# Performance work log

Hardware: AMD Instinct MI355X
Metric: run time of the kernel (lower is better)

## Reference

```python
import jax, jax.numpy as jnp
import numpy as np

D_MODEL = 1024
D_FFN = 4096
H = 16
D_HEAD = D_MODEL // H
B, L = 2, 2048
EPS = 1e-6


def layer_norm(x, a, b):
    # Matches torch: std is unbiased (ddof=1), and divides by (std + eps)
    mean = jnp.mean(x, axis=-1, keepdims=True)
    var = jnp.sum((x - mean) ** 2, axis=-1, keepdims=True) / (x.shape[-1] - 1)
    std = jnp.sqrt(var)
    return (x - mean) / (std + EPS) * a + b


def setup_inputs() -> dict:
    key = jax.random.key(0)
    ks = jax.random.split(key, 10)
    s = 0.02
    x = jax.random.normal(ks[0], (B, L, D_MODEL), dtype=jnp.float32)
    mask = jnp.tril(jnp.ones((L, L), dtype=jnp.int32))[None, None]  # causal [1,1,L,L]
    return {
        "x": x,
        "mask": mask,
        "Wqkv": jax.random.normal(ks[1], (D_MODEL, 3 * D_MODEL), jnp.float32) * s,
        "bqkv": jnp.zeros((3 * D_MODEL,), jnp.float32),
        "Wo": jax.random.normal(ks[2], (D_MODEL, D_MODEL), jnp.float32) * s,
        "bo": jnp.zeros((D_MODEL,), jnp.float32),
        "W1": jax.random.normal(ks[3], (D_MODEL, D_FFN), jnp.float32) * s,
        "b1": jnp.zeros((D_FFN,), jnp.float32),
        "W2": jax.random.normal(ks[4], (D_FFN, D_MODEL), jnp.float32) * s,
        "b2": jnp.zeros((D_MODEL,), jnp.float32),
        "ln1_a": jnp.ones((D_MODEL,), jnp.float32),
        "ln1_b": jnp.zeros((D_MODEL,), jnp.float32),
        "ln2_a": jnp.ones((D_MODEL,), jnp.float32),
        "ln2_b": jnp.zeros((D_MODEL,), jnp.float32),
    }


def reference(x, mask, Wqkv, bqkv, Wo, bo, W1, b1, W2, b2, ln1_a, ln1_b, ln2_a, ln2_b):
    b, l, d = x.shape
    # --- attention sublayer ---
    qkv = x @ Wqkv + bqkv                                   # [b, l, 3*d]
    qkv = qkv.reshape(b, l, 3, H, D_HEAD)                   # '(three h d)' ordering
    q, k, v = qkv[:, :, 0], qkv[:, :, 1], qkv[:, :, 2]      # each [b, l, h, dh]
    scores = jnp.einsum('bqhd,bkhd->bhqk', q, k) / jnp.sqrt(
        jnp.asarray(D_HEAD, x.dtype))                        # [b, h, lq, lk]
    scores = jnp.where(mask == 0, -jnp.inf, scores)
    p = jax.nn.softmax(scores, axis=-1)
    attn = jnp.einsum('bhqk,bkhd->bqhd', p, v).reshape(b, l, d)
    attn_out = attn @ Wo + bo
    x = layer_norm(x + attn_out, ln1_a, ln1_b)
    # --- MLP sublayer ---
    h = jax.nn.relu(x @ W1 + b1)
    mlp_out = h @ W2 + b2
    return layer_norm(x + mlp_out, ln2_a, ln2_b)
```

## Files before the change

### kernel.cpp

```cpp
#include <hip/hip_runtime.h>

#define D_MODEL 1024
#define D_FFN   4096
#define NH      16
#define DH      64
#define BB      2
#define LL      2048
#define MROWS   (BB * LL)

typedef unsigned short u16;
typedef unsigned int   u32;
typedef short bf16x8 __attribute__((ext_vector_type(8)));
typedef float f32x4  __attribute__((ext_vector_type(4)));

__device__ __forceinline__ float bf2f(u16 u) {
    union { u32 i; float f; } v;
    v.i = ((u32)u) << 16;
    return v.f;
}
__device__ __forceinline__ u16 f2bf(float f) {
    union { float f; u32 i; } v;
    v.f = f;
    u32 x = v.i;
    x += 0x7fffu + ((x >> 16) & 1u);
    return (u16)(x >> 16);
}
__device__ __forceinline__ u32 pack_bf_trunc(float a, float b) {
    return __builtin_amdgcn_perm(__float_as_uint(b), __float_as_uint(a),
                                 0x07060302u);
}

typedef const __attribute__((address_space(1))) u32 gu32;
typedef __attribute__((address_space(3))) u32 lu32;
__device__ __forceinline__ void gload_lds16(const void* g, void* l) {
    __builtin_amdgcn_global_load_lds((gu32*)g, (lu32*)l, 16, 0, 0);
}

__device__ __forceinline__ void wt_tile(
    const float* __restrict__ W, u16* __restrict__ Wt,
    int K, int N, int t, int tid, float* tile )
{
    const int ntiles = N >> 6;
    const int n0 = (t % ntiles) * 64;
    const int k0 = (t / ntiles) * 64;

    int kr = tid >> 4;
    int nc = (tid & 15) * 4;
    #pragma unroll
    for (int p = 0; p < 4; ++p) {
        float4 v = *(const float4*)&W[(size_t)(k0 + kr + p * 16) * N + n0 + nc];
        tile[(kr + p * 16) * 65 + nc + 0] = v.x;
        tile[(kr + p * 16) * 65 + nc + 1] = v.y;
        tile[(kr + p * 16) * 65 + nc + 2] = v.z;
        tile[(kr + p * 16) * 65 + nc + 3] = v.w;
    }
    __syncthreads();

    int nr = tid >> 2;
    int kc = (tid & 3) * 16;
    u16 o[16];
    #pragma unroll
    for (int j = 0; j < 16; ++j) o[j] = f2bf(tile[(kc + j) * 65 + nr]);
    u16* dst = &Wt[(size_t)(n0 + nr) * K + k0 + kc];
    *(uint4*)dst       = *(const uint4*)&o[0];
    *(uint4*)(dst + 8) = *(const uint4*)&o[8];
}

__global__ __launch_bounds__(256) void prep_kernel(
    const float* __restrict__ x,    u16* __restrict__ xb,
    const float* __restrict__ Wqkv, u16* __restrict__ Wqkvt)
{
    __shared__ float tile[64 * 65];
    const int tid = threadIdx.x;
    const int bi  = blockIdx.x;

    if (bi < 2048) {
        int i = bi * 2048 + tid * 8;
        float4 a = *(const float4*)(x + i);
        float4 b = *(const float4*)(x + i + 4);
        u16 o[8] = {f2bf(a.x), f2bf(a.y), f2bf(a.z), f2bf(a.w),
                    f2bf(b.x), f2bf(b.y), f2bf(b.z), f2bf(b.w)};
        *(uint4*)(xb + i) = *(const uint4*)o;
        return;
    }
    wt_tile(Wqkv, Wqkvt, 1024, 3072, bi - 2048, tid, tile);
}

template <int EPI, int RF32, int OF32, int KS>
__global__ __launch_bounds__(256, 4) void gemm_bt_kernel(
    const u16* __restrict__ A, const u16* __restrict__ Bt,
    const float* __restrict__ bias, const void* __restrict__ resv,
    void* __restrict__ out0v, u16* __restrict__ out1, u16* __restrict__ out2,
    int M, int N, int K)
{
    __shared__ u16 smem[16384];
    u16* sA = smem;
    u16* sB = smem + 8192;

    const int tid  = threadIdx.x;
    const int lane = tid & 63;
    const int wave = tid >> 6;
    const int wm   = (wave & 1) * 64;
    const int wn   = (wave >> 1) * 64;
    const int quad = lane >> 4;
    const int l16  = lane & 15;

    const int nb  = gridDim.x;
    const int mb  = gridDim.y;
    const int f   = blockIdx.y * nb + blockIdx.x;
    const int xcd = f & 7;
    const int idx = f >> 3;
    const int rn  = nb >> 1;
    const int rm  = mb >> 2;
    const int n0  = ((xcd & 1) * rn + (idx % rn)) * 128;
    const int ym  = (xcd >> 1) * rm + (idx / rn);

    int s, m0;
    if (KS > 1) {
        const int mt = mb / KS;
        s  = ym / mt;
        m0 = (ym % mt) * 128;
    } else {
        s  = 0;
        m0 = ym * 128;
    }
    const int Kseg = K / KS;
    const int kbeg = s * Kseg;

    f32x4 acc[4][4];
    #pragma unroll
    for (int i = 0; i < 4; ++i)
        #pragma unroll
        for (int j = 0; j < 4; ++j)
            acc[i][j] = (f32x4){0.f, 0.f, 0.f, 0.f};

    const u16* Ablk = A  + (size_t)m0 * K;
    const u16* Bblk = Bt + (size_t)n0 * K;

    for (int k0 = kbeg; k0 < kbeg + Kseg; k0 += 64) {
        #pragma unroll
        for (int i = 0; i < 4; ++i) {
            int chunk = (i * 4 + wave) * 64 + lane;
            int r = chunk >> 3;
            int c = (chunk & 7) ^ (r & 7);
            size_t goff = (size_t)r * K + k0 + c * 8;
            gload_lds16(Ablk + goff, &sA[(i * 4 + wave) * 512]);
            gload_lds16(Bblk + goff, &sB[(i * 4 + wave) * 512]);
        }
        __syncthreads();

        #pragma unroll
        for (int ks = 0; ks < 2; ++ks) {
            bf16x8 af[4], bfr[4];
            #pragma unroll
            for (int i = 0; i < 4; ++i) {
                int R = wm + i * 16 + l16;
                int slot = R * 8 + ((ks * 4 + quad) ^ (R & 7));
                af[i] = *(const bf16x8*)&sA[slot * 8];
            }
            #pragma unroll
            for (int j = 0; j < 4; ++j) {
                int R = wn + j * 16 + l16;
                int slot = R * 8 + ((ks * 4 + quad) ^ (R & 7));
                bfr[j] = *(const bf16x8*)&sB[slot * 8];
            }
            #pragma unroll
            for (int i = 0; i < 4; ++i)
                #pragma unroll
                for (int j = 0; j < 4; ++j)
                    acc[i][j] = __builtin_amdgcn_mfma_f32_16x16x32_bf16(
                        af[i], bfr[j], acc[i][j], 0, 0, 0);
        }
        __syncthreads();
    }

    if (EPI == 0 && n0 >= 2 * D_MODEL) {
        u16* tile = smem;
        #pragma unroll
        for (int i = 0; i < 4; ++i) {
            int rl = wm + i * 16 + quad * 4;
            #pragma unroll
            for (int j = 0; j < 4; ++j) {
                int cl = wn + j * 16 + l16;
                float bv = bias[n0 + cl];
                int sx = 8 * (cl & 15);
                #pragma unroll
                for (int r = 0; r < 4; ++r)
                    tile[cl * 128 + ((rl + r) ^ sx)] = f2bf(acc[i][j][r] + bv);
            }
        }
        __syncthreads();
        int cl  = tid >> 1;
        int rb  = (tid & 1) * 64;
        int col = n0 + cl;
        int h   = (col >> 6) & 15;
        int d   = col & 63;
        int b   = m0 >> 11;
        int l0  = (m0 & 2047) + rb;
        int sx  = 8 * (cl & 15);
        u16* dst = out2 + ((size_t)(b * NH + h) * DH + d) * LL + l0;
        #pragma unroll
        for (int u = 0; u < 8; ++u) {
            uint4 q = *(const uint4*)&tile[cl * 128 + ((rb + 8 * u) ^ sx)];
            *(uint4*)(dst + 8 * u) = q;
        }
        return;
    }

    #pragma unroll
    for (int i = 0; i < 4; ++i) {
        int rowb = m0 + wm + i * 16 + quad * 4;
        #pragma unroll
        for (int j = 0; j < 4; ++j) {
            int col = n0 + wn + j * 16 + l16;
            float bv = (EPI == 3) ? 0.f : bias[col];
            #pragma unroll
            for (int r = 0; r < 4; ++r) {
                int rr = rowb + r;
                float v = acc[i][j][r] + bv;
                if (EPI == 0) {
                    int h     = (col >> 6) & 15;
                    int d     = col & 63;
                    int b     = rr >> 11;
                    int l     = rr & 2047;
                    size_t idx2 = ((size_t)(b * NH + h) * LL + l) * DH + d;
                    u16* o0 = (u16*)out0v;
                    if (col < D_MODEL)  o0[idx2]   = f2bf(v * 0.18033688f);
                    else                out1[idx2] = f2bf(v);
                } else if (EPI == 3) {
                    ((u16*)out0v)[((size_t)s * M + rr) * N + col] = f2bf(v);
                } else {
                    size_t idx2 = (size_t)rr * N + col;
                    if (EPI == 1) {
                        v += RF32 ? ((const float*)resv)[idx2]
                                  : bf2f(((const u16*)resv)[idx2]);
                    } else {
                        v = v > 0.f ? v : 0.f;
                    }
                    if (OF32) ((float*)out0v)[idx2] = v;
                    else      ((u16*)out0v)[idx2]   = f2bf(v);
                }
            }
        }
    }
}

template <int EPI, int KS>
__global__ __launch_bounds__(512, 2) void gemm256_kernel(
    const u16* __restrict__ A, const u16* __restrict__ Bt,
    const float* __restrict__ bias, void* __restrict__ outv,
    int M, int N, int K)
{
    __shared__ u16 dsm[65536];

    const int tid  = threadIdx.x;
    const int lane = tid & 63;
    const int wave = tid >> 6;
    const int wm   = wave >> 2;
    const int wn   = wave & 3;
    const int quad = lane >> 4;
    const int l16  = lane & 15;

    const int nb  = gridDim.x;
    const int mb  = gridDim.y;
    const int f   = blockIdx.y * nb + blockIdx.x;
    const int xcd = f & 7;
    const int idx = f >> 3;
    const int rn  = nb >> 1;
    const int rm  = mb >> 2;
    const int n0  = ((xcd & 1) * rn + (idx % rn)) * 256;
    const int ym  = (xcd >> 1) * rm + (idx / rn);

    int s, m0;
    if (KS > 1) {
        const int mt = mb / KS;
        s  = ym / mt;
        m0 = (ym % mt) * 256;
    } else {
        s  = 0;
        m0 = ym * 256;
    }
    const int Kseg = K / KS;
    const int kbeg = s * Kseg;
    const int NT   = Kseg >> 6;

    const int rr = tid >> 3;
    const int cc = ((tid & 7) ^ (rr & 7)) * 8;
    const u16* Asrc[4];
    const u16* Bsrc[4];
    #pragma unroll
    for (int q = 0; q < 4; ++q) {
        Asrc[q] = A  + (size_t)(m0 + q * 64 + rr) * K + kbeg + cc;
        Bsrc[q] = Bt + (size_t)(n0 + q * 64 + rr) * K + kbeg + cc;
    }

    f32x4 acc[8][4];
    #pragma unroll
    for (int i = 0; i < 8; ++i)
        #pragma unroll
        for (int j = 0; j < 4; ++j)
            acc[i][j] = (f32x4){0.f, 0.f, 0.f, 0.f};

    #pragma unroll
    for (int q = 0; q < 4; ++q) {
        gload_lds16(Asrc[q], &dsm[q * 4096 + wave * 512]);
        gload_lds16(Bsrc[q], &dsm[16384 + q * 4096 + wave * 512]);
    }

    #pragma unroll 1
    for (int kt = 0; kt < NT; ++kt) {
        u16* nbuf = &dsm[((kt + 1) & 1) * 32768];
        if (kt + 1 < NT) {
            int koff = (kt + 1) * 64;
            #pragma unroll
            for (int q = 0; q < 4; ++q) {
                gload_lds16(Asrc[q] + koff, nbuf + q * 4096 + wave * 512);
                gload_lds16(Bsrc[q] + koff, nbuf + 16384 + q * 4096 + wave * 512);
            }
            asm volatile("s_waitcnt vmcnt(8)" ::: "memory");
        } else {
            asm volatile("s_waitcnt vmcnt(0)" ::: "memory");
        }
        asm volatile("s_barrier" ::: "memory");
        __builtin_amdgcn_sched_barrier(0);

        const u16* sAc = &dsm[(kt & 1) * 32768];
        const u16* sBc = sAc + 16384;
        #pragma unroll
        for (int ks = 0; ks < 2; ++ks) {
            bf16x8 af[8], bfr[4];
            #pragma unroll
            for (int i = 0; i < 8; ++i) {
                int R = wm * 128 + i * 16 + l16;
                af[i] = *(const bf16x8*)&sAc[(R * 8 + ((ks * 4 + quad) ^ (l16 & 7))) * 8];
            }
            #pragma unroll
            for (int j = 0; j < 4; ++j) {
                int R = wn * 64 + j * 16 + l16;
                bfr[j] = *(const bf16x8*)&sBc[(R * 8 + ((ks * 4 + quad) ^ (l16 & 7))) * 8];
            }
            #pragma unroll
            for (int i = 0; i < 8; ++i)
                #pragma unroll
                for (int j = 0; j < 4; ++j)
                    acc[i][j] = __builtin_amdgcn_mfma_f32_16x16x32_bf16(
                        af[i], bfr[j], acc[i][j], 0, 0, 0);
        }
        __builtin_amdgcn_sched_barrier(0);
        asm volatile("s_barrier" ::: "memory");
    }

    #pragma unroll
    for (int i = 0; i < 8; ++i) {
        int rowb = m0 + wm * 128 + i * 16 + quad * 4;
        #pragma unroll
        for (int j = 0; j < 4; ++j) {
            int col = n0 + wn * 64 + j * 16 + l16;
            float bv = (EPI == 3) ? 0.f : bias[col];
            #pragma unroll
            for (int r = 0; r < 4; ++r) {
                float v = acc[i][j][r] + bv;
                if (EPI == 2) {
                    v = v > 0.f ? v : 0.f;
                    ((u16*)outv)[(size_t)(rowb + r) * N + col] = f2bf(v);
                } else {
                    ((u16*)outv)[((size_t)s * M + rowb + r) * N + col] = f2bf(v);
                }
            }
        }
    }
}

template <int KS, int RF32, int OF32>
__global__ __launch_bounds__(256) void lnfuse_kernel(
    const u16* __restrict__ P, const float* __restrict__ bias,
    const void* __restrict__ resv,
    const float* __restrict__ ga, const float* __restrict__ gb,
    void* __restrict__ outv)
{
    __shared__ float red[8];
    const int tid  = threadIdx.x;
    const int lane = tid & 63;
    const int wave = tid >> 6;
    const size_t row = blockIdx.x;
    const size_t SL  = (size_t)MROWS * D_MODEL;
    const int c = tid * 4;

    float v0, v1, v2, v3;
    {
        float4 bv = *(const float4*)(bias + c);
        v0 = bv.x; v1 = bv.y; v2 = bv.z; v3 = bv.w;
    }
    #pragma unroll
    for (int s = 0; s < KS; ++s) {
        uint2 p = *(const uint2*)(P + s * SL + row * D_MODEL + c);
        v0 += bf2f((u16)p.x); v1 += bf2f((u16)(p.x >> 16));
        v2 += bf2f((u16)p.y); v3 += bf2f((u16)(p.y >> 16));
    }
    if (RF32) {
        float4 r = *(const float4*)((const float*)resv + row * D_MODEL + c);
        v0 += r.x; v1 += r.y; v2 += r.z; v3 += r.w;
    } else {
        uint2 r = *(const uint2*)((const u16*)resv + row * D_MODEL + c);
        v0 += bf2f((u16)r.x); v1 += bf2f((u16)(r.x >> 16));
        v2 += bf2f((u16)r.y); v3 += bf2f((u16)(r.y >> 16));
    }

    float s_ = v0 + v1 + v2 + v3;
    #pragma unroll
    for (int o = 32; o > 0; o >>= 1) s_ += __shfl_xor(s_, o, 64);
    if (lane == 0) red[wave] = s_;
    __syncthreads();
    float mean = (red[0] + red[1] + red[2] + red[3]) * (1.f / 1024.f);

    float d0 = v0 - mean, d1 = v1 - mean, d2 = v2 - mean, d3 = v3 - mean;
    float q = d0 * d0 + d1 * d1 + d2 * d2 + d3 * d3;
    #pragma unroll
    for (int o = 32; o > 0; o >>= 1) q += __shfl_xor(q, o, 64);
    if (lane == 0) red[4 + wave] = q;
    __syncthreads();
    float var = (red[4] + red[5] + red[6] + red[7]) * (1.f / 1023.f);
    float inv = 1.f / (sqrtf(var) + 1e-6f);

    float y0 = d0 * inv * ga[c + 0] + gb[c + 0];
    float y1 = d1 * inv * ga[c + 1] + gb[c + 1];
    float y2 = d2 * inv * ga[c + 2] + gb[c + 2];
    float y3 = d3 * inv * ga[c + 3] + gb[c + 3];
    if (OF32) {
        float4 y = {y0, y1, y2, y3};
        *(float4*)((float*)outv + row * D_MODEL + c) = y;
    } else {
        ushort4 y = {f2bf(y0), f2bf(y1), f2bf(y2), f2bf(y3)};
        *(ushort4*)((u16*)outv + row * D_MODEL + c) = y;
    }
}

__global__ __launch_bounds__(256) void attn_kernel(
    const u16* __restrict__ Q, const u16* __restrict__ K,
    const u16* __restrict__ V, u16* __restrict__ out,
    const float* __restrict__ Wo, u16* __restrict__ Wot,
    const float* __restrict__ W1, u16* __restrict__ W1t,
    const float* __restrict__ W2, u16* __restrict__ W2t)
{
    __shared__ u16 smem[13824];
    u16* ks = smem;
    u16* vs = smem + 4608;
    u16* ps = smem + 9216;

    const int tid  = threadIdx.x;
    const int bi   = blockIdx.x;

    if (bi >= 1024) {
        float* tile = (float*)smem;
        int t = bi - 1024;
        if (t < 256)       wt_tile(Wo, Wot, 1024, 1024, t,        tid, tile);
        else if (t < 1280) wt_tile(W1, W1t, 1024, 4096, t - 256,  tid, tile);
        else               wt_tile(W2, W2t, 4096, 1024, t - 1280, tid, tile);
        return;
    }

    const int lane = tid & 63;
    const int wave = tid >> 6;
    const int l16  = lane & 15;
    const int quad = lane >> 4;

    const int xcd = bi & 7;
    const int idx = bi >> 3;
    const int bh  = xcd * 4 + (idx & 3);
    const int j   = idx >> 2;
    const int qt  = (j < 16) ? (31 - j) : (j - 16);
    const int b   = bh >> 4, h = bh & 15;
    const size_t head_off = (size_t)bh * LL * DH;

    const u16* Qh = Q + head_off;
    const u16* Kh = K + head_off;
    const u16* Vh = V + head_off;

    const int base = qt * 64 + wave * 16;
    const int qg   = base + l16;

    const bf16x8 qf0 = *(const bf16x8*)&Qh[(size_t)qg * DH + quad * 8];
    const bf16x8 qf1 = *(const bf16x8*)&Qh[(size_t)qg * DH + 32 + quad * 8];

    float lsum = 0.f;
    f32x4 o[4];
    #pragma unroll
    for (int t = 0; t < 4; ++t) o[t] = (f32x4){0.f, 0.f, 0.f, 0.f};

    u16* psw = ps + wave * 1152;

    const int key = tid >> 2;
    const int kd0 = (tid & 3) * 16;

    const int vC    = 4 * ((key >> 3) & 7);
    const int vbase = (kd0 >> 1) ^ (vC & 24);
    const int vofA  = vbase + (vC & 4);
    const int vofB  = vbase + ((vC & 4) ^ 4);
    u32* vs32 = (u32*)vs;

    uint4 kr0, kr1, vr0, vr1;
    {
        const u16* ksrc = Kh + (size_t)key * DH + kd0;
        kr0 = *(const uint4*)ksrc;
        kr1 = *(const uint4*)(ksrc + 8);
        const u16* vsrc = Vh + (size_t)key * LL + kd0;
        vr0 = *(const uint4*)vsrc;
        vr1 = *(const uint4*)(vsrc + 8);
    }

    for (int c = 0; c <= qt; ++c) {
        __syncthreads();
        *(uint4*)&ks[key * 72 + kd0]     = kr0;
        *(uint4*)&ks[key * 72 + kd0 + 8] = kr1;
        *(uint4*)&vs32[key * 36 + vofA]  = vr0;
        *(uint4*)&vs32[key * 36 + vofB]  = vr1;
        __syncthreads();
        if (c < qt) {
            const u16* ksrc = Kh + (size_t)((c + 1) * 64 + key) * DH + kd0;
            kr0 = *(const uint4*)ksrc;
            kr1 = *(const uint4*)(ksrc + 8);
            const u16* vsrc = Vh + (size_t)key * LL + (c + 1) * 64 + kd0;
            vr0 = *(const uint4*)vsrc;
            vr1 = *(const uint4*)(vsrc + 8);
        }

        f32x4 st[4];
        #pragma unroll
        for (int t = 0; t < 4; ++t) {
            bf16x8 k0 = *(const bf16x8*)&ks[(t * 16 + l16) * 72 + quad * 8];
            bf16x8 k1 = *(const bf16x8*)&ks[(t * 16 + l16) * 72 + 32 + quad * 8];
            f32x4 s = (f32x4){0.f, 0.f, 0.f, 0.f};
            s = __builtin_amdgcn_mfma_f32_16x16x32_bf16(k0, qf0, s, 0, 0, 0);
            s = __builtin_amdgcn_mfma_f32_16x16x32_bf16(k1, qf1, s, 0, 0, 0);
            st[t] = s;
        }

        if (c == qt) {
            #pragma unroll
            for (int t = 0; t < 4; ++t)
                #pragma unroll
                for (int r = 0; r < 4; ++r)
                    if (c * 64 + t * 16 + quad * 4 + r > qg) st[t][r] = -INFINITY;
        }

        {
            float psum = 0.f;
            #pragma unroll
            for (int t = 0; t < 4; ++t) {
                float p0 = exp2f(st[t][0]), p1 = exp2f(st[t][1]);
                float p2 = exp2f(st[t][2]), p3 = exp2f(st[t][3]);
                psum += (p0 + p1) + (p2 + p3);
                uint2 w = {pack_bf_trunc(p0, p1), pack_bf_trunc(p2, p3)};
                *(uint2*)&psw[l16 * 72 + t * 16 + quad * 4] = w;
            }
            psum += __shfl_xor(psum, 16, 64);
            psum += __shfl_xor(psum, 32, 64);
            lsum += psum;
        }

        bf16x8 pf0 = *(const bf16x8*)&psw[l16 * 72 + quad * 8];
        bf16x8 pf1 = *(const bf16x8*)&psw[l16 * 72 + 32 + quad * 8];

        #pragma unroll
        for (int dt = 0; dt < 4; ++dt) {
            int d  = dt * 16 + l16;
            int sw = 4 * ((d >> 3) & 7);
            bf16x8 vf0 = *(const bf16x8*)&vs[d * 72 + 2 * ((quad * 4) ^ sw)];
            bf16x8 vf1 = *(const bf16x8*)&vs[d * 72 + 2 * ((16 + quad * 4) ^ sw)];
            o[dt] = __builtin_amdgcn_mfma_f32_16x16x32_bf16(pf0, vf0, o[dt], 0, 0, 0);
            o[dt] = __builtin_amdgcn_mfma_f32_16x16x32_bf16(pf1, vf1, o[dt], 0, 0, 0);
        }
    }

    {
        float i0 = 1.f / __shfl(lsum, quad * 4 + 0, 64);
        float i1 = 1.f / __shfl(lsum, quad * 4 + 1, 64);
        float i2 = 1.f / __shfl(lsum, quad * 4 + 2, 64);
        float i3 = 1.f / __shfl(lsum, quad * 4 + 3, 64);
        #pragma unroll
        for (int dt = 0; dt < 4; ++dt) {
            size_t col = h * DH + dt * 16 + l16;
            size_t r0  = ((size_t)b * LL + base + quad * 4) * D_MODEL + col;
            out[r0]               = f2bf(o[dt][0] * i0);
            out[r0 + D_MODEL]     = f2bf(o[dt][1] * i1);
            out[r0 + 2 * D_MODEL] = f2bf(o[dt][2] * i2);
            out[r0 + 3 * D_MODEL] = f2bf(o[dt][3] * i3);
        }
    }
}

extern "C" void kernel_launch(void* const* d_in, const int* in_sizes, int n_in,
                              void* d_out, int out_size, void* d_ws, size_t ws_size,
                              hipStream_t stream)
{
    const float* x    = (const float*)d_in[0];
    const float* Wqkv = (const float*)d_in[2];
    const float* bqkv = (const float*)d_in[3];
    const float* Wo   = (const float*)d_in[4];
    const float* bo   = (const float*)d_in[5];
    const float* W1   = (const float*)d_in[6];
    const float* b1   = (const float*)d_in[7];
    const float* W2   = (const float*)d_in[8];
    const float* b2   = (const float*)d_in[9];
    const float* ln1a = (const float*)d_in[10];
    const float* ln1b = (const float*)d_in[11];
    const float* ln2a = (const float*)d_in[12];
    const float* ln2b = (const float*)d_in[13];

    char* ws = (char*)d_ws;
    const size_t HSZ = (size_t)BB * NH * LL * DH;
    u16*   Qp    = (u16*)ws;
    u16*   Kp    = Qp + HSZ;
    u16*   Vp    = Kp + HSZ;
    u16*   attn  = Vp + HSZ;
    u16*   hbuf  = (u16*)ws;
    u16*   xb    = (u16*)(ws + 33554432);
    u16*   x1    = (u16*)(ws + 50331648);
    u16*   Wqkvt = (u16*)(ws + 58720256);
    u16*   Wot   = (u16*)(ws + 65011712);
    u16*   W1t   = (u16*)(ws + 67108864);
    u16*   W2t   = (u16*)(ws + 75497472);
    u16*   Pbuf  = (u16*)(ws + 83886080);

    dim3 blk(256);

    prep_kernel<<<dim3(2816), blk, 0, stream>>>(x, xb, Wqkv, Wqkvt);

    gemm_bt_kernel<0,0,0,1><<<dim3(24, 32), blk, 0, stream>>>(
        xb, Wqkvt, bqkv, nullptr, Qp, Kp, Vp, MROWS, 3 * D_MODEL, D_MODEL);
    attn_kernel<<<dim3(3328), blk, 0, stream>>>(
        Qp, Kp, Vp, attn, Wo, Wot, W1, W1t, W2, W2t);
    gemm_bt_kernel<3,0,0,2><<<dim3(8, 64), blk, 0, stream>>>(
        attn, Wot, bo, nullptr, Pbuf, nullptr, nullptr, MROWS, D_MODEL, D_MODEL);
    lnfuse_kernel<2,1,0><<<dim3(MROWS), blk, 0, stream>>>(
        Pbuf, bo, x, ln1a, ln1b, x1);
    gemm256_kernel<2,1><<<dim3(16, 16), dim3(512), 0, stream>>>(
        x1, W1t, b1, hbuf, MROWS, D_FFN, D_MODEL);
    gemm256_kernel<3,4><<<dim3(4, 64), dim3(512), 0, stream>>>(
        hbuf, W2t, nullptr, Pbuf, MROWS, D_MODEL, D_FFN);
    lnfuse_kernel<4,0,1><<<dim3(MROWS), blk, 0, stream>>>(
        Pbuf, b2, x1, ln2a, ln2b, d_out);
}
```

Measured before the change: 314.0 us.

## Split GEMM k-tile into four phases interleaving LDS reads, prefetch and MFMA

Restructures the main loop of the 256x256 GEMM into four sub-phases. Each phase loads half the A fragments (plus B when needed) from LDS, issues a quarter of the next tile's global-to-LDS prefetch, then runs 16 MFMAs under raised wave priority (s_setprio). The aim is to overlap global loads and LDS reads with matrix work and to cut register pressure by holding 4 A fragments instead of 8. The cost is more barriers per k-tile, and the full vmcnt(0) wait at the end of each iteration may expose global-load latency.

Measured after the change: 323.2 us. 1.03x slower.

```diff
diff --git a/kernel.cpp b/kernel.cpp
--- a/kernel.cpp
+++ b/kernel.cpp
@@ -260,6 +260,8 @@
     const int wn   = wave & 3;
     const int quad = lane >> 4;
     const int l16  = lane & 15;
+    const int sw0  = quad ^ (l16 & 7);
+    const int sw1  = (4 + quad) ^ (l16 & 7);
 
     const int nb  = gridDim.x;
     const int mb  = gridDim.y;
@@ -306,47 +308,120 @@
         gload_lds16(Asrc[q], &dsm[q * 4096 + wave * 512]);
         gload_lds16(Bsrc[q], &dsm[16384 + q * 4096 + wave * 512]);
     }
+    asm volatile("s_waitcnt vmcnt(0)" ::: "memory");
+    asm volatile("s_barrier" ::: "memory");
 
     #pragma unroll 1
     for (int kt = 0; kt < NT; ++kt) {
-        u16* nbuf = &dsm[((kt + 1) & 1) * 32768];
-        if (kt + 1 < NT) {
-            int koff = (kt + 1) * 64;
-            #pragma unroll
-            for (int q = 0; q < 4; ++q) {
-                gload_lds16(Asrc[q] + koff, nbuf + q * 4096 + wave * 512);
-                gload_lds16(Bsrc[q] + koff, nbuf + 16384 + q * 4096 + wave * 512);
-            }
-            asm volatile("s_waitcnt vmcnt(8)" ::: "memory");
-        } else {
-            asm volatile("s_waitcnt vmcnt(0)" ::: "memory");
-        }
-        asm volatile("s_barrier" ::: "memory");
-        __builtin_amdgcn_sched_barrier(0);
-
         const u16* sAc = &dsm[(kt & 1) * 32768];
         const u16* sBc = sAc + 16384;
-        #pragma unroll
-        for (int ks = 0; ks < 2; ++ks) {
-            bf16x8 af[8], bfr[4];
-            #pragma unroll
-            for (int i = 0; i < 8; ++i) {
-                int R = wm * 128 + i * 16 + l16;
-                af[i] = *(const bf16x8*)&sAc[(R * 8 + ((ks * 4 + quad) ^ (l16 & 7))) * 8];
-            }
-            #pragma unroll
-            for (int j = 0; j < 4; ++j) {
-                int R = wn * 64 + j * 16 + l16;
-                bfr[j] = *(const bf16x8*)&sBc[(R * 8 + ((ks * 4 + quad) ^ (l16 & 7))) * 8];
-            }
-            #pragma unroll
-            for (int i = 0; i < 8; ++i)
-                #pragma unroll
-                for (int j = 0; j < 4; ++j)
-                    acc[i][j] = __builtin_amdgcn_mfma_f32_16x16x32_bf16(
-                        af[i], bfr[j], acc[i][j], 0, 0, 0);
-        }
+        u16* nbuf = &dsm[((kt + 1) & 1) * 32768];
+        const bool pf = (kt + 1 < NT);
+        const int koff = (kt + 1) * 64;
+
+        bf16x8 af[4], bfr[4];
+
+        #pragma unroll
+        for (int i = 0; i < 4; ++i) {
+            int R = wm * 128 + i * 16 + l16;
+            af[i] = *(const bf16x8*)&sAc[(R * 8 + sw0) * 8];
+        }
+        #pragma unroll
+        for (int j = 0; j < 4; ++j) {
+            int R = wn * 64 + j * 16 + l16;
+            bfr[j] = *(const bf16x8*)&sBc[(R * 8 + sw0) * 8];
+        }
+        if (pf) {
+            gload_lds16(Asrc[0] + koff, nbuf + wave * 512);
+            gload_lds16(Asrc[1] + koff, nbuf + 4096 + wave * 512);
+        }
+        asm volatile("s_barrier" ::: "memory");
+        asm volatile("s_waitcnt lgkmcnt(0)" ::: "memory");
         __builtin_amdgcn_sched_barrier(0);
+        __builtin_amdgcn_s_setprio(1);
+        #pragma unroll
+        for (int i = 0; i < 4; ++i)
+            #pragma unroll
+            for (int j = 0; j < 4; ++j)
+                acc[i][j] = __builtin_amdgcn_mfma_f32_16x16x32_bf16(
+                    af[i], bfr[j], acc[i][j], 0, 0, 0);
+        __builtin_amdgcn_s_setprio(0);
+        __builtin_amdgcn_sched_barrier(0);
+        asm volatile("s_barrier" ::: "memory");
+
+        #pragma unroll
+        for (int i = 0; i < 4; ++i) {
+            int R = wm * 128 + (4 + i) * 16 + l16;
+            af[i] = *(const bf16x8*)&sAc[(R * 8 + sw0) * 8];
+        }
+        if (pf) {
+            gload_lds16(Asrc[2] + koff, nbuf + 2 * 4096 + wave * 512);
+            gload_lds16(Asrc[3] + koff, nbuf + 3 * 4096 + wave * 512);
+        }
+        asm volatile("s_barrier" ::: "memory");
+        asm volatile("s_waitcnt lgkmcnt(0)" ::: "memory");
+        __builtin_amdgcn_sched_barrier(0);
+        __builtin_amdgcn_s_setprio(1);
+        #pragma unroll
+        for (int i = 0; i < 4; ++i)
+            #pragma unroll
+            for (int j = 0; j < 4; ++j)
+                acc[4 + i][j] = __builtin_amdgcn_mfma_f32_16x16x32_bf16(
+                    af[i], bfr[j], acc[4 + i][j], 0, 0, 0);
+        __builtin_amdgcn_s_setprio(0);
+        __builtin_amdgcn_sched_barrier(0);
+        asm volatile("s_barrier" ::: "memory");
+
+        #pragma unroll
+        for (int i = 0; i < 4; ++i) {
+            int R = wm * 128 + i * 16 + l16;
+            af[i] = *(const bf16x8*)&sAc[(R * 8 + sw1) * 8];
+        }
+        #pragma unroll
+        for (int j = 0; j < 4; ++j) {
+            int R = wn * 64 + j * 16 + l16;
+            bfr[j] = *(const bf16x8*)&sBc[(R * 8 + sw1) * 8];
+        }
+        if (pf) {
+            gload_lds16(Bsrc[0] + koff, nbuf + 16384 + wave * 512);
+            gload_lds16(Bsrc[1] + koff, nbuf + 16384 + 4096 + wave * 512);
+        }
+        asm volatile("s_barrier" ::: "memory");
+        asm volatile("s_waitcnt lgkmcnt(0)" ::: "memory");
+        __builtin_amdgcn_sched_barrier(0);
+        __builtin_amdgcn_s_setprio(1);
+        #pragma unroll
+        for (int i = 0; i < 4; ++i)
+            #pragma unroll
+            for (int j = 0; j < 4; ++j)
+                acc[i][j] = __builtin_amdgcn_mfma_f32_16x16x32_bf16(
+                    af[i], bfr[j], acc[i][j], 0, 0, 0);
+        __builtin_amdgcn_s_setprio(0);
+        __builtin_amdgcn_sched_barrier(0);
+        asm volatile("s_barrier" ::: "memory");
+
+        #pragma unroll
+        for (int i = 0; i < 4; ++i) {
+            int R = wm * 128 + (4 + i) * 16 + l16;
+            af[i] = *(const bf16x8*)&sAc[(R * 8 + sw1) * 8];
+        }
+        if (pf) {
+            gload_lds16(Bsrc[2] + koff, nbuf + 16384 + 2 * 4096 + wave * 512);
+            gload_lds16(Bsrc[3] + koff, nbuf + 16384 + 3 * 4096 + wave * 512);
+        }
+        asm volatile("s_barrier" ::: "memory");
+        asm volatile("s_waitcnt lgkmcnt(0)" ::: "memory");
+        __builtin_amdgcn_sched_barrier(0);
+        __builtin_amdgcn_s_setprio(1);
+        #pragma unroll
+        for (int i = 0; i < 4; ++i)
+            #pragma unroll
+            for (int j = 0; j < 4; ++j)
+                acc[4 + i][j] = __builtin_amdgcn_mfma_f32_16x16x32_bf16(
+                    af[i], bfr[j], acc[4 + i][j], 0, 0, 0);
+        __builtin_amdgcn_s_setprio(0);
+        __builtin_amdgcn_sched_barrier(0);
+        asm volatile("s_waitcnt vmcnt(0)" ::: "memory");
         asm volatile("s_barrier" ::: "memory");
     }
 
```

## Switch gemm256 to triple-buffered BK=32 pipeline with MFMA priority boost

Applied to the files above, without the earlier changes.

Reworks the 256x256 GEMM main loop from a double-buffered K-tile of 64 to a triple-buffered K-tile of 32, prefetching two stages ahead, and shrinks LDS from 128KB to 96KB. LDS swizzle and global load mapping are adjusted for the narrower 32-element rows. It adds an explicit lgkmcnt wait before the MFMA block and raises wave priority during the MFMAs. The aim is deeper latency hiding of global loads. In exchange it doubles the number of barriers per K and gives each iteration less work between syncs.

Result: slower. 320.5 us (+2.1%).

```diff
diff --git a/kernel.cpp b/kernel.cpp
--- a/kernel.cpp
+++ b/kernel.cpp
@@ -251,7 +251,7 @@
     const float* __restrict__ bias, void* __restrict__ outv,
     int M, int N, int K)
 {
-    __shared__ u16 dsm[65536];
+    __shared__ u16 dsm[49152];
 
     const int tid  = threadIdx.x;
     const int lane = tid & 63;
@@ -282,16 +282,16 @@
     }
     const int Kseg = K / KS;
     const int kbeg = s * Kseg;
-    const int NT   = Kseg >> 6;
-
-    const int rr = tid >> 3;
-    const int cc = ((tid & 7) ^ (rr & 7)) * 8;
-    const u16* Asrc[4];
-    const u16* Bsrc[4];
-    #pragma unroll
-    for (int q = 0; q < 4; ++q) {
-        Asrc[q] = A  + (size_t)(m0 + q * 64 + rr) * K + kbeg + cc;
-        Bsrc[q] = Bt + (size_t)(n0 + q * 64 + rr) * K + kbeg + cc;
+    const int NT   = Kseg >> 5;
+
+    const int rr2 = tid >> 2;
+    const int cc  = ((tid & 3) ^ (rr2 & 3)) * 8;
+    const u16* Asrc[2];
+    const u16* Bsrc[2];
+    #pragma unroll
+    for (int q = 0; q < 2; ++q) {
+        Asrc[q] = A  + (size_t)(m0 + q * 128 + rr2) * K + kbeg + cc;
+        Bsrc[q] = Bt + (size_t)(n0 + q * 128 + rr2) * K + kbeg + cc;
     }
 
     f32x4 acc[8][4];
@@ -301,53 +301,61 @@
         for (int j = 0; j < 4; ++j)
             acc[i][j] = (f32x4){0.f, 0.f, 0.f, 0.f};
 
-    #pragma unroll
-    for (int q = 0; q < 4; ++q) {
-        gload_lds16(Asrc[q], &dsm[q * 4096 + wave * 512]);
-        gload_lds16(Bsrc[q], &dsm[16384 + q * 4096 + wave * 512]);
-    }
-
+    auto STAGE = [&](int t, int b) {
+        const int koff = t * 32;
+        u16* bb = &dsm[b * 16384];
+        #pragma unroll
+        for (int q = 0; q < 2; ++q)
+            gload_lds16(Asrc[q] + koff, bb + q * 4096 + wave * 512);
+        #pragma unroll
+        for (int q = 0; q < 2; ++q)
+            gload_lds16(Bsrc[q] + koff, bb + 8192 + q * 4096 + wave * 512);
+    };
+
+    STAGE(0, 0);
+    STAGE(1, 1);
+
+    int bc = 0;
+    int bs = 2;
     #pragma unroll 1
     for (int kt = 0; kt < NT; ++kt) {
-        u16* nbuf = &dsm[((kt + 1) & 1) * 32768];
-        if (kt + 1 < NT) {
-            int koff = (kt + 1) * 64;
-            #pragma unroll
-            for (int q = 0; q < 4; ++q) {
-                gload_lds16(Asrc[q] + koff, nbuf + q * 4096 + wave * 512);
-                gload_lds16(Bsrc[q] + koff, nbuf + 16384 + q * 4096 + wave * 512);
-            }
+        if (kt + 2 < NT) {
+            STAGE(kt + 2, bs);
             asm volatile("s_waitcnt vmcnt(8)" ::: "memory");
+        } else if (kt + 1 < NT) {
+            asm volatile("s_waitcnt vmcnt(4)" ::: "memory");
         } else {
             asm volatile("s_waitcnt vmcnt(0)" ::: "memory");
         }
         asm volatile("s_barrier" ::: "memory");
+
+        const u16* sAc = &dsm[bc * 16384];
+        const u16* sBc = sAc + 8192;
+        bf16x8 af[8], bfr[4];
+        #pragma unroll
+        for (int i = 0; i < 8; ++i) {
+            int R = wm * 128 + i * 16 + l16;
+            af[i] = *(const bf16x8*)&sAc[(R * 4 + (quad ^ (R & 3))) * 8];
+        }
+        #pragma unroll
+        for (int j = 0; j < 4; ++j) {
+            int R = wn * 64 + j * 16 + l16;
+            bfr[j] = *(const bf16x8*)&sBc[(R * 4 + (quad ^ (R & 3))) * 8];
+        }
+        asm volatile("s_waitcnt lgkmcnt(0)" ::: "memory");
         __builtin_amdgcn_sched_barrier(0);
-
-        const u16* sAc = &dsm[(kt & 1) * 32768];
-        const u16* sBc = sAc + 16384;
-        #pragma unroll
-        for (int ks = 0; ks < 2; ++ks) {
-            bf16x8 af[8], bfr[4];
-            #pragma unroll
-            for (int i = 0; i < 8; ++i) {
-                int R = wm * 128 + i * 16 + l16;
-                af[i] = *(const bf16x8*)&sAc[(R * 8 + ((ks * 4 + quad) ^ (l16 & 7))) * 8];
-            }
-            #pragma unroll
-            for (int j = 0; j < 4; ++j) {
-                int R = wn * 64 + j * 16 + l16;
-                bfr[j] = *(const bf16x8*)&sBc[(R * 8 + ((ks * 4 + quad) ^ (l16 & 7))) * 8];
-            }
-            #pragma unroll
-            for (int i = 0; i < 8; ++i)
-                #pragma unroll
-                for (int j = 0; j < 4; ++j)
-                    acc[i][j] = __builtin_amdgcn_mfma_f32_16x16x32_bf16(
-                        af[i], bfr[j], acc[i][j], 0, 0, 0);
-        }
+        __builtin_amdgcn_s_setprio(1);
+        #pragma unroll
+        for (int i = 0; i < 8; ++i)
+            #pragma unroll
+            for (int j = 0; j < 4; ++j)
+                acc[i][j] = __builtin_amdgcn_mfma_f32_16x16x32_bf16(
+                    af[i], bfr[j], acc[i][j], 0, 0, 0);
+        __builtin_amdgcn_s_setprio(0);
         __builtin_amdgcn_sched_barrier(0);
         asm volatile("s_barrier" ::: "memory");
+        bc = (bc == 2) ? 0 : bc + 1;
+        bs = (bs == 2) ? 0 : bs + 1;
     }
 
     #pragma unroll
```
